# Optimization experiments

Measured on AMD Instinct MI355X. Metric: run time of the kernel, lower is better.

The kernel has to match this reference:

```python
import jax, jax.numpy as jnp
import numpy as np

B, N, C = 2, 20000, 256
TEST_MAX_BOX = 5000
IOU_THRESHOLDS = (0.4, 0.6, 0.8)
N_HIDDEN_LAYERS = 6  # six Conv1d(256,256,k=1)+LeakyReLU blocks in mask_w_layers


def setup_inputs() -> dict:
    key = jax.random.key(0)
    ks = jax.random.split(key, 8)
    # valid xyxy boxes: top-left in [0,900), w/h in [4,84)
    xy = jax.random.uniform(ks[0], (B, 2, N), dtype=jnp.float32) * 900.0
    wh = jax.random.uniform(ks[1], (B, 2, N), dtype=jnp.float32) * 80.0 + 4.0
    box = jnp.concatenate([xy, xy + wh], axis=1)              # [B,4,N]
    score = jax.random.uniform(ks[2], (B, 1, N), dtype=jnp.float32)
    feat = jax.random.normal(ks[3], (B, C, N), dtype=jnp.float32)
    W = jax.random.normal(ks[4], (N_HIDDEN_LAYERS, C, C), dtype=jnp.float32) * 0.02
    b = jnp.zeros((N_HIDDEN_LAYERS, C), dtype=jnp.float32)
    Wf = jax.random.normal(ks[5], (len(IOU_THRESHOLDS), C), dtype=jnp.float32) * 0.02
    bf = jnp.zeros((len(IOU_THRESHOLDS),), dtype=jnp.float32)
    return {"box": box, "score": score, "feat": feat, "W": W, "b": b, "Wf": Wf, "bf": bf}


def _box_iou(a, bxs):
    # a: [N,4], bxs: [M,4], xyxy -> [N,M] (torchvision ops.box_iou)
    area_a = (a[:, 2] - a[:, 0]) * (a[:, 3] - a[:, 1])
    area_b = (bxs[:, 2] - bxs[:, 0]) * (bxs[:, 3] - bxs[:, 1])
    lt = jnp.maximum(a[:, None, :2], bxs[None, :, :2])
    rb = jnp.minimum(a[:, None, 2:], bxs[None, :, 2:])
    wh = jnp.clip(rb - lt, 0.0)
    inter = wh[..., 0] * wh[..., 1]
    return inter / (area_a[:, None] + area_b[None, :] - inter)


def reference(box, score, feat, W, b, Wf, bf):
    # forward_test path of LMM
    boxT = jnp.swapaxes(box, 1, 2)                 # [B,N,4]
    s = jnp.swapaxes(score, 1, 2)[..., 0]          # [B,N]
    top_s, keep = jax.lax.top_k(s, TEST_MAX_BOX)   # [B,K] each, sorted desc
    boxK = jnp.take_along_axis(boxT, keep[..., None], axis=1)   # [B,K,4]
    featK = jnp.take_along_axis(feat, keep[:, None, :], axis=2)  # [B,C,K]

    iou = jax.vmap(_box_iou)(boxK, boxK)           # [B,K,K]
    idx = jnp.arange(TEST_MAX_BOX)
    masks = []
    for thr in IOU_THRESHOLDS:
        adjc = jnp.where(iou >= thr, 1.0, 0.0) * top_s[:, :, None]  # [B,K,K]
        max_idx = jnp.argmax(adjc, axis=1)                           # [B,K]
        masks.append((max_idx == idx[None, :]).astype(featK.dtype))
    masks = jnp.stack(masks, axis=1)               # [B,3,K]

    x = featK
    for l in range(N_HIDDEN_LAYERS):
        x = jax.nn.leaky_relu(jnp.einsum('oi,bik->bok', W[l], x) + b[l][:, None], 0.2)
    mask_w = jax.nn.softmax(jnp.einsum('oi,bik->bok', Wf, x) + bf[:, None], axis=1)  # [B,3,K]

    loc_max = jnp.sum(masks * mask_w, axis=1, keepdims=True)  # [B,1,K]
    return (loc_max, keep)
```

## Files before the change

kernel.cpp:

```cpp
#include <hip/hip_runtime.h>

#define B_  2
#define N_  20000
#define C_  256
#define K_  5000
#define M_  (B_ * K_)
#define CAP_ 5376
#define NBIN_ 2048
#define AST_ 264
#define RT_  21
#define RCH_ 7
#define RCT_ 3

typedef __attribute__((ext_vector_type(8))) short bf16x8;
typedef __attribute__((ext_vector_type(4))) float f32x4;
typedef __attribute__((ext_vector_type(2))) unsigned long long ull2;

__device__ __forceinline__ unsigned short f2bf(float x) {
  unsigned u = __float_as_uint(x);
  return (unsigned short)((u + 0x7fffu + ((u >> 16) & 1u)) >> 16);
}
__device__ __forceinline__ unsigned fkey(float f) {
  unsigned u = __float_as_uint(f);
  return (u & 0x80000000u) ? ~u : (u | 0x80000000u);
}
__device__ __forceinline__ int binof(float s) {
  int b = (int)(s * 2048.0f);
  return b < 0 ? 0 : (b > 2047 ? 2047 : b);
}
__device__ __forceinline__ bf16x8 as_bf(uint4 v) {
  union { uint4 u; bf16x8 b; } c; c.u = v; return c.b;
}

__global__ __launch_bounds__(256) void k_prep(const float* __restrict__ W,
                                              const float* __restrict__ score,
                                              unsigned short* __restrict__ Whi,
                                              int* __restrict__ nc,
                                              int* __restrict__ cnt2,
                                              int* __restrict__ selb) {
  const int u = blockIdx.x;
  const int t = threadIdx.x;
  if (u >= 192) {
    if (u == 234) { if (t < B_) nc[t] = 0; return; }
    if (u >= 235) {
      const int b = u - 235;
      __shared__ int h[NBIN_];
      __shared__ int chs[256];
      const float* s = score + b * N_;
      for (int i = t; i < NBIN_; i += 256) h[i] = 0;
      __syncthreads();
      for (int i = t; i < N_ / 4; i += 256) {
        const float4 v = ((const float4*)s)[i];
        atomicAdd(&h[binof(v.x)], 1);
        atomicAdd(&h[binof(v.y)], 1);
        atomicAdd(&h[binof(v.z)], 1);
        atomicAdd(&h[binof(v.w)], 1);
      }
      __syncthreads();
      int sum = 0;
#pragma unroll
      for (int j = 0; j < 8; ++j) sum += h[t * 8 + j];
      chs[t] = sum;
      __syncthreads();
      for (int off = 1; off < 256; off <<= 1) {
        int v = chs[t] + ((t + off < 256) ? chs[t + off] : 0);
        __syncthreads();
        chs[t] = v;
        __syncthreads();
      }
      const int above = (t + 1 < 256) ? chs[t + 1] : 0;
      if (above < K_ && K_ <= chs[t]) {
        int acc = above;
        for (int i = 7; i >= 0; --i) {
          const int bin = t * 8 + i;
          if (acc + h[bin] >= K_) { selb[b] = bin; break; }
          acc += h[bin];
        }
      }
      return;
    }
    const int i = (u - 192) * 256 + t;
    if (i < B_ * CAP_) cnt2[i] = 0;
    return;
  }
  const int idx = u * 256 + t;
  const int lane = idx & 63;
  const int oi = (idx >> 6) & 1;
  const int ks = (idx >> 7) & 7;
  const int w = (idx >> 10) & 7;
  const int l = idx >> 13;
  const int o = w * 32 + oi * 16 + (lane & 15);
  const int k0 = ks * 32 + (lane >> 4) * 8;
  const float* src = W + ((size_t)(l * C_ + o)) * C_ + k0;
  float4 w0 = *(const float4*)&src[0];
  float4 w1 = *(const float4*)&src[4];
  const float wv[8] = {w0.x, w0.y, w0.z, w0.w, w1.x, w1.y, w1.z, w1.w};
  unsigned short hs[8];
#pragma unroll
  for (int q = 0; q < 8; ++q) hs[q] = f2bf(wv[q]);
  *(uint4*)&Whi[(size_t)idx * 8] = *(const uint4*)&hs[0];
}

__global__ __launch_bounds__(256) void k_selcomp(const float* __restrict__ score,
                                                 const int* __restrict__ selb,
                                                 int* __restrict__ nc,
                                                 unsigned long long* __restrict__ ck,
                                                 int* __restrict__ rnk) {
  const int b = blockIdx.y;
  const float* s = score + b * N_;
  const int selB = selb[b];
  const int n = blockIdx.x * 256 + threadIdx.x;
  if (n < N_) {
    rnk[b * N_ + n] = K_;
    const float sv = s[n];
    if (binof(sv) >= selB) {
      const int pos = atomicAdd(&nc[b], 1);
      if (pos < CAP_)
        ck[b * CAP_ + pos] =
            ((unsigned long long)fkey(sv) << 32) | (unsigned)(N_ - 1 - n);
    }
  }
}

__global__ __launch_bounds__(256) void k_rank2(const int* __restrict__ nc,
                                               const unsigned long long* __restrict__ ck,
                                               int* __restrict__ cnt2) {
  const int b = blockIdx.z;
  int S = nc[b]; if (S > CAP_) S = CAP_;
  __shared__ unsigned long long sk[256];
  const int t = threadIdx.x;
  const int j = blockIdx.x * 256 + t;
  const unsigned long long* kb = ck + b * CAP_;
  const unsigned long long myk = (j < S) ? kb[j] : 0ULL;
  int c = 0;
  const int nt = (S + 255) >> 8;
  int t0 = blockIdx.y * RCT_, t1 = t0 + RCT_;
  if (t1 > nt) t1 = nt;
  for (int tt = t0; tt < t1; ++tt) {
    const int gi = tt * 256 + t;
    unsigned long long kk = (gi < S) ? kb[gi] : 0ULL;
    __syncthreads();
    sk[t] = kk;
    __syncthreads();
#pragma unroll 8
    for (int ii = 0; ii < 256; ii += 2) {
      ull2 v = *(const ull2*)&sk[ii];
      c += (int)(v.x > myk) + (int)(v.y > myk);
    }
  }
  if (j < S && c > 0) atomicAdd(&cnt2[b * CAP_ + j], c);
}

__global__ __launch_bounds__(256) void k_scatter2(const int* __restrict__ nc,
                                                  const unsigned long long* __restrict__ ck,
                                                  const int* __restrict__ cnt2,
                                                  const float* __restrict__ box,
                                                  int* __restrict__ keep_i,
                                                  float* __restrict__ out_keep,
                                                  int* __restrict__ rnk,
                                                  float* __restrict__ boxK,
                                                  unsigned* __restrict__ maxiou) {
  const int b = blockIdx.y;
  int S = nc[b]; if (S > CAP_) S = CAP_;
  const int j = blockIdx.x * 256 + threadIdx.x;
  if (j >= S) return;
  const int c = cnt2[b * CAP_ + j];
  if (c >= K_) return;
  const int n = N_ - 1 - (int)(ck[b * CAP_ + j] & 0xffffffffu);
  keep_i[b * K_ + c] = n;
  out_keep[b * K_ + c] = (float)n;
  rnk[b * N_ + n] = c;
  const float* bb = box + (size_t)b * 4 * N_;
  float4 v;
  v.x = bb[n]; v.y = bb[N_ + n]; v.z = bb[2 * N_ + n]; v.w = bb[3 * N_ + n];
  ((float4*)boxK)[b * K_ + c] = v;
  maxiou[b * K_ + c] = 0u;
}

__global__ __launch_bounds__(256) void k_ioug(const float* __restrict__ boxK,
                                              unsigned* __restrict__ maxiou,
                                              const int* __restrict__ rnk,
                                              const float* __restrict__ feat,
                                              unsigned short* __restrict__ Xhi) {
  __shared__ __align__(16) char arena[16640];
  const int u = blockIdx.x;
  const int t = threadIdx.x;
  if (u < 420) {
    const int b = u / 210;
    const int p = u % 210;
    int jt = 0;
    while ((jt + 1) * (jt + 2) / 2 <= p) ++jt;
    const int it = p - jt * (jt + 1) / 2;
    float* sx0 = (float*)arena;
    float* sy0 = sx0 + 256; float* sx1 = sy0 + 256;
    float* sy1 = sx1 + 256; float* sa = sy1 + 256;
    const int gi0 = it * 256;
    const int gl = gi0 + t;
    if (gl < K_) {
      float4 v = ((const float4*)boxK)[b * K_ + gl];
      sx0[t] = v.x; sy0[t] = v.y; sx1[t] = v.z; sy1[t] = v.w;
      sa[t] = __fmul_rn(__fsub_rn(v.z, v.x), __fsub_rn(v.w, v.y));
    } else {
      sx0[t] = 1e30f; sy0[t] = 1e30f; sx1[t] = -1e30f; sy1[t] = -1e30f;
      sa[t] = 0.f;
    }
    __syncthreads();
    const int j = jt * 256 + t;
    if (j >= K_) return;
    float4 v = ((const float4*)boxK)[b * K_ + j];
    const float aj = __fmul_rn(__fsub_rn(v.z, v.x), __fsub_rn(v.w, v.y));
    float mx = 0.f;
    int lim = j - gi0;
    if (lim > 256) lim = 256;
    for (int ii = 0; ii < lim; ++ii) {
      float ltx = fmaxf(sx0[ii], v.x);
      float lty = fmaxf(sy0[ii], v.y);
      float rbx = fminf(sx1[ii], v.z);
      float rby = fminf(sy1[ii], v.w);
      float wx = fmaxf(__fsub_rn(rbx, ltx), 0.f);
      float wy = fmaxf(__fsub_rn(rby, lty), 0.f);
      float inter = __fmul_rn(wx, wy);
      if (inter > 0.f) {
        float uni = __fsub_rn(__fadd_rn(sa[ii], aj), inter);
        mx = fmaxf(mx, __fdiv_rn(inter, uni));
      }
    }
    if (mx > 0.f) atomicMax(&maxiou[b * K_ + j], __float_as_uint(mx));
  } else {
    const int v2 = u - 420;
    const int b = v2 / 1252;
    const int rem = v2 % 1252;
    const int c0 = (rem / 313) * 64;
    const int n0 = (rem % 313) * 64;
    float* T = (float*)arena;
    const int nl = t & 63, wq = t >> 6;
#pragma unroll
    for (int r = 0; r < 16; ++r) {
      const int cl = r * 4 + wq;
      const int n = n0 + nl;
      T[nl * 65 + cl] =
          (n < N_) ? feat[((size_t)(b * C_ + c0 + cl)) * N_ + n] : 0.f;
    }
    __syncthreads();
    const int nn = n0 + (t >> 2);
    if (nn >= N_) return;
    const int r = rnk[b * N_ + nn];
    if (r >= K_) return;
    const int cseg = (t & 3) * 16;
    unsigned short hb[16];
#pragma unroll
    for (int i = 0; i < 16; ++i)
      hb[i] = f2bf(T[(t >> 2) * 65 + cseg + i]);
    const size_t base = (size_t)(b * K_ + r) * C_ + c0 + cseg;
    *(uint4*)&Xhi[base] = *(const uint4*)&hb[0];
    *(uint4*)&Xhi[base + 8] = *(const uint4*)&hb[8];
  }
}

__global__ __launch_bounds__(512, 2) void k_mlp6(
    const unsigned short* __restrict__ Whi,
    const float* __restrict__ bias, const float* __restrict__ Wf,
    const float* __restrict__ bf, const unsigned* __restrict__ maxiou,
    const unsigned short* __restrict__ Xhi,
    float* __restrict__ out_loc) {
  __shared__ __align__(16) unsigned short act_hi[32 * AST_];
  __shared__ float swf[768];
  const int t = threadIdx.x;
  const int m0 = blockIdx.x * 32;

  {
    const int r = t >> 4;
    const int cs = (t & 15) * 16;
    const size_t g = (size_t)(m0 + r) * C_ + cs;
    *(uint4*)&act_hi[r * AST_ + cs] = *(const uint4*)&Xhi[g];
    *(uint4*)&act_hi[r * AST_ + cs + 8] = *(const uint4*)&Xhi[g + 8];
  }
  for (int i = t; i < 768; i += 512) swf[i] = Wf[i];
  __syncthreads();

  const int lane = t & 63;
  const int w = t >> 6;
  const int quad = lane >> 4, l15 = lane & 15;

  for (int l = 0; l < 6; ++l) {
    const size_t wbase = (size_t)(l * 8 + w) * 8192 + (size_t)lane * 8;
    f32x4 acc[2][2];
#pragma unroll
    for (int oi = 0; oi < 2; ++oi)
#pragma unroll
      for (int mi = 0; mi < 2; ++mi) acc[oi][mi] = (f32x4)0.f;
    uint4 nwh[2];
#pragma unroll
    for (int oi = 0; oi < 2; ++oi)
      nwh[oi] = *(const uint4*)&Whi[wbase + oi * 512];
#pragma unroll
    for (int ks = 0; ks < 8; ++ks) {
      bf16x8 wh[2];
#pragma unroll
      for (int oi = 0; oi < 2; ++oi) wh[oi] = as_bf(nwh[oi]);
      if (ks < 7) {
        const size_t nb = wbase + (size_t)(ks + 1) * 1024;
#pragma unroll
        for (int oi = 0; oi < 2; ++oi)
          nwh[oi] = *(const uint4*)&Whi[nb + oi * 512];
      }
      bf16x8 Ah[2];
#pragma unroll
      for (int mi = 0; mi < 2; ++mi)
        Ah[mi] = *(const bf16x8*)&act_hi[(mi * 16 + l15) * AST_ + ks * 32 + quad * 8];
#pragma unroll
      for (int mi = 0; mi < 2; ++mi)
#pragma unroll
        for (int oi = 0; oi < 2; ++oi)
          acc[oi][mi] = __builtin_amdgcn_mfma_f32_16x16x32_bf16(wh[oi], Ah[mi], acc[oi][mi], 0, 0, 0);
    }
    __syncthreads();
    const int o0 = w * 32 + quad * 4;
#pragma unroll
    for (int oi = 0; oi < 2; ++oi) {
      const float4 bb = *(const float4*)&bias[l * C_ + o0 + oi * 16];
#pragma unroll
      for (int mi = 0; mi < 2; ++mi) {
        float y0 = acc[oi][mi][0] + bb.x; y0 = fmaxf(y0, 0.2f * y0);
        float y1 = acc[oi][mi][1] + bb.y; y1 = fmaxf(y1, 0.2f * y1);
        float y2 = acc[oi][mi][2] + bb.z; y2 = fmaxf(y2, 0.2f * y2);
        float y3 = acc[oi][mi][3] + bb.w; y3 = fmaxf(y3, 0.2f * y3);
        uint2 pk;
        pk.x = (unsigned)f2bf(y0) | ((unsigned)f2bf(y1) << 16);
        pk.y = (unsigned)f2bf(y2) | ((unsigned)f2bf(y3) << 16);
        *(uint2*)&act_hi[(mi * 16 + l15) * AST_ + o0 + oi * 16] = pk;
      }
    }
    __syncthreads();
  }

  const int r = t >> 4;
  const int part = t & 15;
  const int m = m0 + r;
  float a0 = 0.f, a1 = 0.f, a2 = 0.f;
  for (int c = part * 16; c < part * 16 + 16; c += 2) {
    const unsigned hv = *(const unsigned*)&act_hi[r * AST_ + c];
    const float x0 = __uint_as_float((hv & 0xffffu) << 16);
    const float x1 = __uint_as_float(hv & 0xffff0000u);
    a0 += swf[c] * x0 + swf[c + 1] * x1;
    a1 += swf[256 + c] * x0 + swf[256 + c + 1] * x1;
    a2 += swf[512 + c] * x0 + swf[512 + c + 1] * x1;
  }
#pragma unroll
  for (int off = 1; off < 16; off <<= 1) {
    a0 += __shfl_xor(a0, off);
    a1 += __shfl_xor(a1, off);
    a2 += __shfl_xor(a2, off);
  }
  if (part == 0 && m < M_) {
    a0 += bf[0]; a1 += bf[1]; a2 += bf[2];
    const float mxv = fmaxf(a0, fmaxf(a1, a2));
    const float e0 = expf(a0 - mxv);
    const float e1 = expf(a1 - mxv);
    const float e2 = expf(a2 - mxv);
    const float inv = 1.f / (e0 + e1 + e2);
    const float miou = __uint_as_float(maxiou[m]);
    float loc = 0.f;
    if (miou < 0.4f) loc += e0;
    if (miou < 0.6f) loc += e1;
    if (miou < 0.8f) loc += e2;
    out_loc[m] = loc * inv;
  }
}

extern "C" void kernel_launch(void* const* d_in, const int* in_sizes, int n_in,
                              void* d_out, int out_size, void* d_ws, size_t ws_size,
                              hipStream_t stream) {
  const float* box   = (const float*)d_in[0];
  const float* score = (const float*)d_in[1];
  const float* feat  = (const float*)d_in[2];
  const float* W     = (const float*)d_in[3];
  const float* bias  = (const float*)d_in[4];
  const float* Wf    = (const float*)d_in[5];
  const float* bf    = (const float*)d_in[6];

  float* out = (float*)d_out;
  float* out_loc  = out;
  float* out_keep = out + M_;

  char* ws = (char*)d_ws;
  int*            keep_i = (int*)(ws + 0);
  float*          boxK   = (float*)(ws + 40960);
  unsigned*       maxiou = (unsigned*)(ws + 201216);
  unsigned short* Whi    = (unsigned short*)(ws + 241664);
  unsigned short* XtA_hi = (unsigned short*)(ws + 1814528);
  int*                rnk    = (int*)(ws + 12169216);
  unsigned long long* ck     = (unsigned long long*)(ws + 12329216);
  int*                cnt2   = (int*)(ws + 12415232);
  int*                nc     = (int*)(ws + 12458240);
  int*                selb   = (int*)(ws + 12458248);

  k_prep<<<237, 256, 0, stream>>>(W, score, Whi, nc, cnt2, selb);
  k_selcomp<<<dim3(79, B_), 256, 0, stream>>>(score, selb, nc, ck, rnk);
  k_rank2<<<dim3(RT_, RCH_, B_), 256, 0, stream>>>(nc, ck, cnt2);
  k_scatter2<<<dim3(RT_, B_), 256, 0, stream>>>(nc, ck, cnt2, box, keep_i,
                                                out_keep, rnk, boxK, maxiou);
  k_ioug<<<2924, 256, 0, stream>>>(boxK, maxiou, rnk, feat, XtA_hi);
  k_mlp6<<<313, 512, 0, stream>>>(Whi, bias, Wf, bf, maxiou, XtA_hi, out_loc);
}
```

Measured before the change: 177.3 us.

## Replace O(S^2) rank counting with bucketed counting sort in one block per batch

The global compaction, all-pairs rank counting and scatter kernels are replaced by a single kernel with one 1024-thread block per batch. That kernel reuses the score histogram from the prep kernel to compute per-bin offsets, places candidates into shared memory by bin, and ranks each candidate only against the others in its own bin. This removes two kernel launches, the global atomics and the quadratic comparison work. In exchange the top-k selection runs on only two workgroups, so it depends on bins staying small and could serialize on a skewed score distribution.

```diff
diff --git a/kernel.cpp b/kernel.cpp
--- a/kernel.cpp
+++ b/kernel.cpp
@@ -8,13 +8,9 @@
 #define CAP_ 5376
 #define NBIN_ 2048
 #define AST_ 264
-#define RT_  21
-#define RCH_ 7
-#define RCT_ 3
 
 typedef __attribute__((ext_vector_type(8))) short bf16x8;
 typedef __attribute__((ext_vector_type(4))) float f32x4;
-typedef __attribute__((ext_vector_type(2))) unsigned long long ull2;
 
 __device__ __forceinline__ unsigned short f2bf(float x) {
   unsigned u = __float_as_uint(x);
@@ -35,52 +31,52 @@
 __global__ __launch_bounds__(256) void k_prep(const float* __restrict__ W,
                                               const float* __restrict__ score,
                                               unsigned short* __restrict__ Whi,
-                                              int* __restrict__ nc,
-                                              int* __restrict__ cnt2,
-                                              int* __restrict__ selb) {
+                                              int* __restrict__ selb,
+                                              int* __restrict__ h_glob,
+                                              int* __restrict__ rnk) {
   const int u = blockIdx.x;
   const int t = threadIdx.x;
   if (u >= 192) {
-    if (u == 234) { if (t < B_) nc[t] = 0; return; }
-    if (u >= 235) {
-      const int b = u - 235;
-      __shared__ int h[NBIN_];
-      __shared__ int chs[256];
-      const float* s = score + b * N_;
-      for (int i = t; i < NBIN_; i += 256) h[i] = 0;
+    if (u >= 194) {
+      const int i = (u - 194) * 256 + t;
+      if (i < B_ * N_) rnk[i] = K_;
+      return;
+    }
+    const int b = u - 192;
+    __shared__ int h[NBIN_];
+    __shared__ int chs[256];
+    const float* s = score + b * N_;
+    for (int i = t; i < NBIN_; i += 256) h[i] = 0;
+    __syncthreads();
+    for (int i = t; i < N_ / 4; i += 256) {
+      const float4 v = ((const float4*)s)[i];
+      atomicAdd(&h[binof(v.x)], 1);
+      atomicAdd(&h[binof(v.y)], 1);
+      atomicAdd(&h[binof(v.z)], 1);
+      atomicAdd(&h[binof(v.w)], 1);
+    }
+    __syncthreads();
+    int sum = 0;
+#pragma unroll
+    for (int j = 0; j < 8; ++j) sum += h[t * 8 + j];
+    chs[t] = sum;
+    __syncthreads();
+    for (int off = 1; off < 256; off <<= 1) {
+      int v = chs[t] + ((t + off < 256) ? chs[t + off] : 0);
       __syncthreads();
-      for (int i = t; i < N_ / 4; i += 256) {
-        const float4 v = ((const float4*)s)[i];
-        atomicAdd(&h[binof(v.x)], 1);
-        atomicAdd(&h[binof(v.y)], 1);
-        atomicAdd(&h[binof(v.z)], 1);
-        atomicAdd(&h[binof(v.w)], 1);
-      }
+      chs[t] = v;
       __syncthreads();
-      int sum = 0;
-#pragma unroll
-      for (int j = 0; j < 8; ++j) sum += h[t * 8 + j];
-      chs[t] = sum;
-      __syncthreads();
-      for (int off = 1; off < 256; off <<= 1) {
-        int v = chs[t] + ((t + off < 256) ? chs[t + off] : 0);
-        __syncthreads();
-        chs[t] = v;
-        __syncthreads();
-      }
-      const int above = (t + 1 < 256) ? chs[t + 1] : 0;
-      if (above < K_ && K_ <= chs[t]) {
-        int acc = above;
-        for (int i = 7; i >= 0; --i) {
-          const int bin = t * 8 + i;
-          if (acc + h[bin] >= K_) { selb[b] = bin; break; }
-          acc += h[bin];
-        }
-      }
-      return;
-    }
-    const int i = (u - 192) * 256 + t;
-    if (i < B_ * CAP_) cnt2[i] = 0;
+    }
+    const int above = (t + 1 < 256) ? chs[t + 1] : 0;
+    if (above < K_ && K_ <= chs[t]) {
+      int acc = above;
+      for (int i = 7; i >= 0; --i) {
+        const int bin = t * 8 + i;
+        if (acc + h[bin] >= K_) { selb[b] = bin; break; }
+        acc += h[bin];
+      }
+    }
+    for (int i = t; i < NBIN_; i += 256) h_glob[b * NBIN_ + i] = h[i];
     return;
   }
   const int idx = u * 256 + t;
@@ -101,80 +97,78 @@
   *(uint4*)&Whi[(size_t)idx * 8] = *(const uint4*)&hs[0];
 }
 
-__global__ __launch_bounds__(256) void k_selcomp(const float* __restrict__ score,
-                                                 const int* __restrict__ selb,
-                                                 int* __restrict__ nc,
-                                                 unsigned long long* __restrict__ ck,
-                                                 int* __restrict__ rnk) {
-  const int b = blockIdx.y;
+__global__ __launch_bounds__(1024) void k_rankscatter(
+    const float* __restrict__ score, const int* __restrict__ selb,
+    const int* __restrict__ h_glob, const float* __restrict__ box,
+    int* __restrict__ keep_i, float* __restrict__ out_keep,
+    int* __restrict__ rnk, float* __restrict__ boxK,
+    unsigned* __restrict__ maxiou) {
+  __shared__ int h[NBIN_];
+  __shared__ int sfx[NBIN_];
+  __shared__ int chs[1024];
+  __shared__ unsigned long long sorted[CAP_];
+  const int b = blockIdx.x;
+  const int t = threadIdx.x;
+  const int selB = selb[b];
+  h[t] = h_glob[b * NBIN_ + t];
+  h[t + 1024] = h_glob[b * NBIN_ + t + 1024];
+  __syncthreads();
+  chs[t] = h[2 * t] + h[2 * t + 1];
+  __syncthreads();
+  for (int off = 1; off < 1024; off <<= 1) {
+    int v = chs[t] + ((t + off < 1024) ? chs[t + off] : 0);
+    __syncthreads();
+    chs[t] = v;
+    __syncthreads();
+  }
+  const int above = (t + 1 < 1024) ? chs[t + 1] : 0;
+  sfx[2 * t + 1] = above;
+  sfx[2 * t] = above + h[2 * t + 1];
+  __syncthreads();
+  int S = sfx[selB] + h[selB];
+  if (S > CAP_) S = CAP_;
+  __syncthreads();
+  h[t] = 0; h[t + 1024] = 0;
+  __syncthreads();
   const float* s = score + b * N_;
-  const int selB = selb[b];
-  const int n = blockIdx.x * 256 + threadIdx.x;
-  if (n < N_) {
-    rnk[b * N_ + n] = K_;
-    const float sv = s[n];
-    if (binof(sv) >= selB) {
-      const int pos = atomicAdd(&nc[b], 1);
-      if (pos < CAP_)
-        ck[b * CAP_ + pos] =
-            ((unsigned long long)fkey(sv) << 32) | (unsigned)(N_ - 1 - n);
-    }
-  }
-}
-
-__global__ __launch_bounds__(256) void k_rank2(const int* __restrict__ nc,
-                                               const unsigned long long* __restrict__ ck,
-                                               int* __restrict__ cnt2) {
-  const int b = blockIdx.z;
-  int S = nc[b]; if (S > CAP_) S = CAP_;
-  __shared__ unsigned long long sk[256];
-  const int t = threadIdx.x;
-  const int j = blockIdx.x * 256 + t;
-  const unsigned long long* kb = ck + b * CAP_;
-  const unsigned long long myk = (j < S) ? kb[j] : 0ULL;
-  int c = 0;
-  const int nt = (S + 255) >> 8;
-  int t0 = blockIdx.y * RCT_, t1 = t0 + RCT_;
-  if (t1 > nt) t1 = nt;
-  for (int tt = t0; tt < t1; ++tt) {
-    const int gi = tt * 256 + t;
-    unsigned long long kk = (gi < S) ? kb[gi] : 0ULL;
-    __syncthreads();
-    sk[t] = kk;
-    __syncthreads();
-#pragma unroll 8
-    for (int ii = 0; ii < 256; ii += 2) {
-      ull2 v = *(const ull2*)&sk[ii];
-      c += (int)(v.x > myk) + (int)(v.y > myk);
-    }
-  }
-  if (j < S && c > 0) atomicAdd(&cnt2[b * CAP_ + j], c);
-}
-
-__global__ __launch_bounds__(256) void k_scatter2(const int* __restrict__ nc,
-                                                  const unsigned long long* __restrict__ ck,
-                                                  const int* __restrict__ cnt2,
-                                                  const float* __restrict__ box,
-                                                  int* __restrict__ keep_i,
-                                                  float* __restrict__ out_keep,
-                                                  int* __restrict__ rnk,
-                                                  float* __restrict__ boxK,
-                                                  unsigned* __restrict__ maxiou) {
-  const int b = blockIdx.y;
-  int S = nc[b]; if (S > CAP_) S = CAP_;
-  const int j = blockIdx.x * 256 + threadIdx.x;
-  if (j >= S) return;
-  const int c = cnt2[b * CAP_ + j];
-  if (c >= K_) return;
-  const int n = N_ - 1 - (int)(ck[b * CAP_ + j] & 0xffffffffu);
-  keep_i[b * K_ + c] = n;
-  out_keep[b * K_ + c] = (float)n;
-  rnk[b * N_ + n] = c;
+  for (int i4 = t; i4 < N_ / 4; i4 += 1024) {
+    const float4 v = ((const float4*)s)[i4];
+    const float sv[4] = {v.x, v.y, v.z, v.w};
+#pragma unroll
+    for (int q = 0; q < 4; ++q) {
+      const int bin = binof(sv[q]);
+      if (bin >= selB) {
+        const int pos = sfx[bin] + atomicAdd(&h[bin], 1);
+        if (pos < CAP_) {
+          const int n = i4 * 4 + q;
+          sorted[pos] = ((unsigned long long)fkey(sv[q]) << 32) |
+                        (unsigned)(N_ - 1 - n);
+        }
+      }
+    }
+  }
+  __syncthreads();
   const float* bb = box + (size_t)b * 4 * N_;
-  float4 v;
-  v.x = bb[n]; v.y = bb[N_ + n]; v.z = bb[2 * N_ + n]; v.w = bb[3 * N_ + n];
-  ((float4*)boxK)[b * K_ + c] = v;
-  maxiou[b * K_ + c] = 0u;
+  for (int p = t; p < S; p += 1024) {
+    const unsigned long long k = sorted[p];
+    const unsigned fk = (unsigned)(k >> 32);
+    const unsigned uu = (fk & 0x80000000u) ? (fk & 0x7fffffffu) : ~fk;
+    const int bin = binof(__uint_as_float(uu));
+    const int start = sfx[bin];
+    int end = start + h[bin];
+    if (end > S) end = S;
+    int c = start;
+    for (int q2 = start; q2 < end; ++q2) c += (int)(sorted[q2] > k);
+    if (c >= K_) continue;
+    const int n = N_ - 1 - (int)(k & 0xffffffffu);
+    keep_i[b * K_ + c] = n;
+    out_keep[b * K_ + c] = (float)n;
+    rnk[b * N_ + n] = c;
+    float4 v;
+    v.x = bb[n]; v.y = bb[N_ + n]; v.z = bb[2 * N_ + n]; v.w = bb[3 * N_ + n];
+    ((float4*)boxK)[b * K_ + c] = v;
+    maxiou[b * K_ + c] = 0u;
+  }
 }
 
 __global__ __launch_bounds__(256) void k_ioug(const float* __restrict__ boxK,
@@ -390,16 +384,12 @@
   unsigned short* Whi    = (unsigned short*)(ws + 241664);
   unsigned short* XtA_hi = (unsigned short*)(ws + 1814528);
   int*                rnk    = (int*)(ws + 12169216);
-  unsigned long long* ck     = (unsigned long long*)(ws + 12329216);
-  int*                cnt2   = (int*)(ws + 12415232);
-  int*                nc     = (int*)(ws + 12458240);
-  int*                selb   = (int*)(ws + 12458248);
-
-  k_prep<<<237, 256, 0, stream>>>(W, score, Whi, nc, cnt2, selb);
-  k_selcomp<<<dim3(79, B_), 256, 0, stream>>>(score, selb, nc, ck, rnk);
-  k_rank2<<<dim3(RT_, RCH_, B_), 256, 0, stream>>>(nc, ck, cnt2);
-  k_scatter2<<<dim3(RT_, B_), 256, 0, stream>>>(nc, ck, cnt2, box, keep_i,
-                                                out_keep, rnk, boxK, maxiou);
+  int*                h_glob = (int*)(ws + 12329216);
+  int*                selb   = (int*)(ws + 12345600);
+
+  k_prep<<<351, 256, 0, stream>>>(W, score, Whi, selb, h_glob, rnk);
+  k_rankscatter<<<B_, 1024, 0, stream>>>(score, selb, h_glob, box, keep_i,
+                                         out_keep, rnk, boxK, maxiou);
   k_ioug<<<2924, 256, 0, stream>>>(boxK, maxiou, rnk, feat, XtA_hi);
   k_mlp6<<<313, 512, 0, stream>>>(Whi, bias, Wf, bf, maxiou, XtA_hi, out_loc);
 }
```

After: 178.6 us. About the same (+0.7%).
